# Kernel optimization log

Measured on AMD Instinct MI355X. Metric: run time of the kernel, lower is better.

Reference implementation:

```python
import jax, jax.numpy as jnp
import numpy as np

N_NODES = 100000
N_EDGES = 3200000
IN_DIM = 512
OUT_DIM = 3


def _sage_conv(x, src, dst, ll_w, ll_b, lr_w):
    # PyG SAGEConv (mean aggr): out = lin_l(mean_{j in N(i)} x_j) + lin_r(x_i)
    n = x.shape[0]
    msgs = x[src]                                            # [E, d_in]
    agg = jax.ops.segment_sum(msgs, dst, num_segments=n)      # [N, d_in]
    cnt = jax.ops.segment_sum(jnp.ones((src.shape[0],), x.dtype), dst, num_segments=n)
    mean = agg / jnp.maximum(cnt, 1.0)[:, None]
    return mean @ ll_w + ll_b + x @ lr_w


def setup_inputs() -> dict:
    key = jax.random.key(0)
    ks = jax.random.split(key, 16)
    d = {}
    d["x"] = jax.random.normal(ks[0], (N_NODES, IN_DIM), dtype=jnp.float32)
    d["edge_index"] = jax.random.randint(ks[1], (2, N_EDGES), 0, N_NODES, dtype=jnp.int64)
    s = lambda fan_in: 1.0 / np.sqrt(fan_in)
    d["fc1_w"] = jax.random.uniform(ks[2], (IN_DIM, 16), jnp.float32, -s(IN_DIM), s(IN_DIM))
    d["fc1_b"] = jax.random.uniform(ks[3], (16,), jnp.float32, -s(IN_DIM), s(IN_DIM))
    d["conv1_ll_w"] = jax.random.uniform(ks[4], (16, 32), jnp.float32, -s(16), s(16))
    d["conv1_ll_b"] = jnp.zeros((32,), jnp.float32)
    d["conv1_lr_w"] = jax.random.uniform(ks[5], (16, 32), jnp.float32, -s(16), s(16))
    d["conv2_ll_w"] = jax.random.uniform(ks[6], (32, 16), jnp.float32, -s(32), s(32))
    d["conv2_ll_b"] = jnp.zeros((16,), jnp.float32)
    d["conv2_lr_w"] = jax.random.uniform(ks[7], (32, 16), jnp.float32, -s(32), s(32))
    d["fc2_w"] = jax.random.uniform(ks[8], (16, OUT_DIM), jnp.float32, -s(16), s(16))
    d["fc2_b"] = jax.random.uniform(ks[9], (OUT_DIM,), jnp.float32, -s(16), s(16))
    return d


def reference(x, edge_index, fc1_w, fc1_b, conv1_ll_w, conv1_ll_b, conv1_lr_w,
              conv2_ll_w, conv2_ll_b, conv2_lr_w, fc2_w, fc2_b):
    src, dst = edge_index[0], edge_index[1]
    h = jax.nn.relu(x @ fc1_w + fc1_b)                              # [N, 16]
    h = jax.nn.relu(_sage_conv(h, src, dst, conv1_ll_w, conv1_ll_b, conv1_lr_w))  # [N, 32]
    h = jax.nn.relu(_sage_conv(h, src, dst, conv2_ll_w, conv2_ll_b, conv2_lr_w))  # [N, 16]
    h = h @ fc2_w + fc2_b                                           # [N, 3]
    gsi = jax.nn.sigmoid(h[:, 1])
    mxi = jax.nn.sigmoid(h[:, 2])
    fsi = jax.nn.relu(h[:, 0]) + gsi
    return jnp.stack([fsi, gsi, mxi], axis=1)
```

## Files before the change

### kernel.cpp

```cpp
#include <hip/hip_runtime.h>
#include <math.h>

#define N_NODES 100000
#define N_EDGES 3200000
#define BSHIFT 8
#define NPB 256
#define BMASK (NPB - 1)
#define NB 391
#define CAP 10240
#define STG_BLOCKS 512
#define FC1_BLOCKS 2048
#define NTILES 6250

typedef __attribute__((ext_vector_type(8))) short short8v;
typedef __attribute__((ext_vector_type(4))) float f32x4;
typedef __attribute__((address_space(3))) unsigned lds_u32;
typedef const __attribute__((address_space(1))) unsigned glb_u32;

__device__ inline unsigned cvt_pk_bf16(float a, float b) {
  unsigned r;
  asm("v_cvt_pk_bf16_f32 %0, %1, %2" : "=v"(r) : "v"(a), "v"(b));
  return r;
}
__device__ inline unsigned short f32_to_bf16(float f) {
  union { float f; unsigned u; } v; v.f = f;
  unsigned r = v.u + 0x7fff + ((v.u >> 16) & 1);
  return (unsigned short)(r >> 16);
}
__device__ inline float bf16_to_f32(unsigned short h) {
  union { unsigned u; float f; } v; v.u = ((unsigned)h) << 16;
  return v.f;
}

__global__ __launch_bounds__(256) void fc1_stage_kernel(
    const float* __restrict__ x, const float* __restrict__ w,
    const float* __restrict__ b, unsigned short* __restrict__ h1,
    const int* __restrict__ src, const int* __restrict__ dst,
    int* __restrict__ gcur, int* __restrict__ staged) {
  __shared__ __align__(16) char smem[53248];

  if (blockIdx.x >= STG_BLOCKS) {
    float* tile = (float*)smem;
    short8v (*wlds)[64] = (short8v(*)[64])(smem + 32768);
    f32x4* pbuf = (f32x4*)(smem + 49152);
    const int tid = threadIdx.x;
    const int lane = tid & 63;
    const int wib = tid >> 6;
    const int o = lane & 15;
    const int kb = lane >> 4;

    for (int i = tid; i < 2048; i += 256)
      ((float4*)tile)[i] = ((const float4*)w)[i];
    __syncthreads();
    for (int idx = tid; idx < 4096; idx += 256) {
      const int s = idx >> 8, ln = (idx >> 2) & 63, j = idx & 3;
      const int lkb = ln >> 4, lo = ln & 15;
      const int k = s * 32 + lkb * 8 + 2 * j;
      ((unsigned*)&wlds[s][ln])[j] =
          cvt_pk_bf16(tile[k * 16 + lo], tile[(k + 1) * 16 + lo]);
    }
    __syncthreads();

    const float bias = b[o];
    const int fcb = blockIdx.x - STG_BLOCKS;

    for (int tileid = fcb; tileid < NTILES; tileid += FC1_BLOCKS) {
      const float* xbase = x + (size_t)tileid * 8192;
#pragma unroll
      for (int i = 0; i < 8; ++i) {
        const int c = wib * 8 + i;
        const int r = c >> 1;
        const int off = (c & 1) * 1024 + lane * 16;
        const int goff = off ^ ((r & 7) << 5);
        __builtin_amdgcn_global_load_lds(
            (glb_u32*)(xbase + r * 512 + (goff >> 2)),
            (lds_u32*)((char*)tile + (size_t)c * 1024 + lane * 16) - lane * 4,
            16, 0, 0);
      }
      __syncthreads();

      f32x4 c4 = {0.f, 0.f, 0.f, 0.f};
#pragma unroll
      for (int ss = 0; ss < 4; ++ss) {
        const int s = wib * 4 + ss;
        const int cb = (s * 128 + kb * 32) ^ ((o & 7) << 5);
        const char* p = (const char*)tile + o * 2048 + cb;
        const float4 a0 = *(const float4*)p;
        const float4 a1 = *(const float4*)(p + 16);
        union { unsigned u[4]; short8v v; } fa;
        fa.u[0] = cvt_pk_bf16(a0.x, a0.y);
        fa.u[1] = cvt_pk_bf16(a0.z, a0.w);
        fa.u[2] = cvt_pk_bf16(a1.x, a1.y);
        fa.u[3] = cvt_pk_bf16(a1.z, a1.w);
        c4 = __builtin_amdgcn_mfma_f32_16x16x32_bf16(fa.v, wlds[s][lane], c4,
                                                     0, 0, 0);
      }
      pbuf[wib * 64 + lane] = c4;
      __syncthreads();
      if (wib == 0) {
        const f32x4 p0 = pbuf[lane];
        const f32x4 p1 = pbuf[64 + lane];
        const f32x4 p2 = pbuf[128 + lane];
        const f32x4 p3 = pbuf[192 + lane];
        const int rbase = tileid * 16 + (lane >> 4) * 4;
#pragma unroll
        for (int j = 0; j < 4; ++j) {
          const float vj = (p0[j] + p1[j]) + (p2[j] + p3[j]);
          h1[(size_t)(rbase + j) * 16 + o] =
              f32_to_bf16(fmaxf(vj + bias, 0.f));
        }
      }
      __syncthreads();
    }
  } else {
    int* hist = (int*)smem;
    int* base = (int*)(smem + 2048);
    const int tid = threadIdx.x;
    for (int i = tid; i < NB; i += 256) hist[i] = 0;
    __syncthreads();

    const int sb = blockIdx.x;
    const int per = (N_EDGES + STG_BLOCKS - 1) / STG_BLOCKS;
    const int e0 = sb * per;
    const int e1 = min(e0 + per, N_EDGES);

    for (int e = e0 + tid; e < e1; e += 256) {
      atomicAdd(&hist[dst[e] >> BSHIFT], 1);
    }
    __syncthreads();
    for (int bkt = tid; bkt < NB; bkt += 256) {
      int h = hist[bkt];
      base[bkt] = (h > 0) ? atomicAdd(&gcur[bkt], h) : 0;
      hist[bkt] = 0;
    }
    __syncthreads();
    for (int e = e0 + tid; e < e1; e += 256) {
      int d = dst[e];
      int s = src[e];
      int bkt = d >> BSHIFT;
      int pos = base[bkt] + atomicAdd(&hist[bkt], 1);
      if (pos < CAP) staged[bkt * CAP + pos] = (s << 8) | (d & BMASK);
    }
  }
}

__global__ __launch_bounds__(256) void finalize_kernel(
    int* __restrict__ staged, const int* __restrict__ gcur,
    int* __restrict__ offs, int* __restrict__ cnt) {
  __shared__ int ed[CAP];
  __shared__ int lcnt[NPB];
  __shared__ int lofs[NPB];
  __shared__ int sc[256];
  const int bkt = blockIdx.x, tid = threadIdx.x;
  const int nE = min(gcur[bkt], CAP);
  const int base = bkt * CAP;
  for (int e = tid; e < nE; e += 256) ed[e] = staged[base + e];
  lcnt[tid] = 0;
  __syncthreads();
  for (int e = tid; e < nE; e += 256) atomicAdd(&lcnt[ed[e] & BMASK], 1);
  __syncthreads();
  const int v = lcnt[tid];
  sc[tid] = v;
  __syncthreads();
  for (int d = 1; d < 256; d <<= 1) {
    int add = (tid >= d) ? sc[tid - d] : 0;
    __syncthreads();
    sc[tid] += add;
    __syncthreads();
  }
  const int excl = sc[tid] - v;
  lofs[tid] = excl;
  const int g = bkt * NPB + tid;
  if (g < N_NODES) {
    offs[g] = base + excl;
    cnt[g] = v;
  }
  lcnt[tid] = 0;
  __syncthreads();
  for (int e = tid; e < nE; e += 256) {
    int u = ed[e];
    int dl = u & BMASK;
    int pos = lofs[dl] + atomicAdd(&lcnt[dl], 1);
    staged[base + pos] = u >> 8;
  }
}

__global__ __launch_bounds__(256) void conv1_kernel(
    const unsigned short* __restrict__ h1, const int* __restrict__ csr,
    const int* __restrict__ offs, const int* __restrict__ cnt,
    const float* __restrict__ llw, const float* __restrict__ llb,
    const float* __restrict__ lrw, const float* __restrict__ c2llw,
    float* __restrict__ h2, unsigned short* __restrict__ t2) {
  __shared__ float wl[512], wr[512], w2c[512];
  __shared__ float bb[32];
  for (int idx = threadIdx.x; idx < 512; idx += 256) {
    const int k = idx >> 5, jj = idx & 31;
    const int sj = 4 * ((jj >> 2) ^ (k >> 2)) + (jj & 3);
    wl[k * 32 + sj] = llw[idx];
    wr[k * 32 + sj] = lrw[idx];
    w2c[idx] = c2llw[idx];
  }
  if (threadIdx.x < 32) bb[threadIdx.x] = llb[threadIdx.x];
  __syncthreads();

  const int tid = blockIdx.x * 256 + threadIdx.x;
  const int i = tid >> 3;
  if (i >= N_NODES) return;
  const int t8 = threadIdx.x & 7;
  const int gg = t8 >> 2;
  const int t = t8 & 3;
  const int start = offs[i], deg = cnt[i];

  float4 acc = make_float4(0.f, 0.f, 0.f, 0.f);
  int e = gg;
  for (; e + 6 < deg; e += 8) {
    const int s0 = csr[start + e];
    const int s1 = csr[start + e + 2];
    const int s2 = csr[start + e + 4];
    const int s3 = csr[start + e + 6];
    ushort4 a0 = *(const ushort4*)(h1 + (size_t)s0 * 16 + t * 4);
    ushort4 a1 = *(const ushort4*)(h1 + (size_t)s1 * 16 + t * 4);
    ushort4 a2 = *(const ushort4*)(h1 + (size_t)s2 * 16 + t * 4);
    ushort4 a3 = *(const ushort4*)(h1 + (size_t)s3 * 16 + t * 4);
    acc.x += (bf16_to_f32(a0.x) + bf16_to_f32(a1.x)) +
             (bf16_to_f32(a2.x) + bf16_to_f32(a3.x));
    acc.y += (bf16_to_f32(a0.y) + bf16_to_f32(a1.y)) +
             (bf16_to_f32(a2.y) + bf16_to_f32(a3.y));
    acc.z += (bf16_to_f32(a0.z) + bf16_to_f32(a1.z)) +
             (bf16_to_f32(a2.z) + bf16_to_f32(a3.z));
    acc.w += (bf16_to_f32(a0.w) + bf16_to_f32(a1.w)) +
             (bf16_to_f32(a2.w) + bf16_to_f32(a3.w));
  }
  for (; e < deg; e += 2) {
    const int s = csr[start + e];
    ushort4 a = *(const ushort4*)(h1 + (size_t)s * 16 + t * 4);
    acc.x += bf16_to_f32(a.x); acc.y += bf16_to_f32(a.y);
    acc.z += bf16_to_f32(a.z); acc.w += bf16_to_f32(a.w);
  }
  acc.x += __shfl_xor(acc.x, 4, 64);
  acc.y += __shfl_xor(acc.y, 4, 64);
  acc.z += __shfl_xor(acc.z, 4, 64);
  acc.w += __shfl_xor(acc.w, 4, 64);

  const float inv = 1.f / (float)(deg > 0 ? deg : 1);
  const ushort4 selfu = *(const ushort4*)(h1 + (size_t)i * 16 + t * 4);
  const float mk[4] = {acc.x * inv, acc.y * inv, acc.z * inv, acc.w * inv};
  const float sk[4] = {bf16_to_f32(selfu.x), bf16_to_f32(selfu.y),
                       bf16_to_f32(selfu.z), bf16_to_f32(selfu.w)};

  float4 p[8];
#pragma unroll
  for (int q = 0; q < 8; ++q) p[q] = make_float4(0.f, 0.f, 0.f, 0.f);
#pragma unroll
  for (int j = 0; j < 4; ++j) {
    const int k = 4 * t + j;
#pragma unroll
    for (int q = 0; q < 8; ++q) {
      const int qs = 4 * (q ^ t);
      float4 w4l = *(const float4*)&wl[k * 32 + qs];
      float4 w4r = *(const float4*)&wr[k * 32 + qs];
      p[q].x += mk[j] * w4l.x + sk[j] * w4r.x;
      p[q].y += mk[j] * w4l.y + sk[j] * w4r.y;
      p[q].z += mk[j] * w4l.z + sk[j] * w4r.z;
      p[q].w += mk[j] * w4l.w + sk[j] * w4r.w;
    }
  }
#pragma unroll
  for (int mask = 1; mask <= 2; mask <<= 1) {
#pragma unroll
    for (int q = 0; q < 8; ++q) {
      p[q].x += __shfl_xor(p[q].x, mask, 64);
      p[q].y += __shfl_xor(p[q].y, mask, 64);
      p[q].z += __shfl_xor(p[q].z, mask, 64);
      p[q].w += __shfl_xor(p[q].w, mask, 64);
    }
  }
  float o[32];
#pragma unroll
  for (int q = 0; q < 8; ++q) {
    o[4 * q + 0] = fmaxf(p[q].x + bb[4 * q + 0], 0.f);
    o[4 * q + 1] = fmaxf(p[q].y + bb[4 * q + 1], 0.f);
    o[4 * q + 2] = fmaxf(p[q].z + bb[4 * q + 2], 0.f);
    o[4 * q + 3] = fmaxf(p[q].w + bb[4 * q + 3], 0.f);
  }
  *(float4*)(h2 + (size_t)i * 32 + 4 * t8) =
      make_float4(o[4 * t8], o[4 * t8 + 1], o[4 * t8 + 2], o[4 * t8 + 3]);
  float t0 = 0.f, t1 = 0.f;
#pragma unroll
  for (int k = 0; k < 32; ++k) {
    const float ok = o[k];
    t0 += ok * w2c[k * 16 + 2 * t8];
    t1 += ok * w2c[k * 16 + 2 * t8 + 1];
  }
  *(unsigned*)(t2 + (size_t)i * 16 + 2 * t8) = cvt_pk_bf16(t0, t1);
}

__global__ __launch_bounds__(256) void conv2_kernel(
    const unsigned short* __restrict__ t2, const float* __restrict__ h2,
    const int* __restrict__ csr, const int* __restrict__ offs,
    const int* __restrict__ cnt, const float* __restrict__ llb,
    const float* __restrict__ lrw, const float* __restrict__ fc2w,
    const float* __restrict__ fc2b, float* __restrict__ out) {
  __shared__ float wr[512];
  __shared__ float bb[16];
  __shared__ float w2[48];
  __shared__ float b2[3];
  for (int idx = threadIdx.x; idx < 512; idx += 256) {
    const int k = idx >> 4, jj = idx & 15;
    const int sj = 4 * ((jj >> 2) ^ ((k >> 2) & 3)) + (jj & 3);
    wr[k * 16 + sj] = lrw[idx];
  }
  if (threadIdx.x < 16) bb[threadIdx.x] = llb[threadIdx.x];
  else if (threadIdx.x >= 64 && threadIdx.x < 112) w2[threadIdx.x - 64] = fc2w[threadIdx.x - 64];
  else if (threadIdx.x >= 128 && threadIdx.x < 131) b2[threadIdx.x - 128] = fc2b[threadIdx.x - 128];
  __syncthreads();

  const int tid = blockIdx.x * 256 + threadIdx.x;
  const int i = tid >> 3;
  if (i >= N_NODES) return;
  const int t8 = threadIdx.x & 7;
  const int gg = t8 >> 2;
  const int t = t8 & 3;
  const int start = offs[i], deg = cnt[i];

  float4 acc = make_float4(0.f, 0.f, 0.f, 0.f);
  int e = gg;
  for (; e + 6 < deg; e += 8) {
    const int s0 = csr[start + e];
    const int s1 = csr[start + e + 2];
    const int s2 = csr[start + e + 4];
    const int s3 = csr[start + e + 6];
    ushort4 a0 = *(const ushort4*)(t2 + (size_t)s0 * 16 + t * 4);
    ushort4 a1 = *(const ushort4*)(t2 + (size_t)s1 * 16 + t * 4);
    ushort4 a2 = *(const ushort4*)(t2 + (size_t)s2 * 16 + t * 4);
    ushort4 a3 = *(const ushort4*)(t2 + (size_t)s3 * 16 + t * 4);
    acc.x += (bf16_to_f32(a0.x) + bf16_to_f32(a1.x)) +
             (bf16_to_f32(a2.x) + bf16_to_f32(a3.x));
    acc.y += (bf16_to_f32(a0.y) + bf16_to_f32(a1.y)) +
             (bf16_to_f32(a2.y) + bf16_to_f32(a3.y));
    acc.z += (bf16_to_f32(a0.z) + bf16_to_f32(a1.z)) +
             (bf16_to_f32(a2.z) + bf16_to_f32(a3.z));
    acc.w += (bf16_to_f32(a0.w) + bf16_to_f32(a1.w)) +
             (bf16_to_f32(a2.w) + bf16_to_f32(a3.w));
  }
  for (; e < deg; e += 2) {
    const int s = csr[start + e];
    ushort4 a = *(const ushort4*)(t2 + (size_t)s * 16 + t * 4);
    acc.x += bf16_to_f32(a.x); acc.y += bf16_to_f32(a.y);
    acc.z += bf16_to_f32(a.z); acc.w += bf16_to_f32(a.w);
  }
  acc.x += __shfl_xor(acc.x, 4, 64);
  acc.y += __shfl_xor(acc.y, 4, 64);
  acc.z += __shfl_xor(acc.z, 4, 64);
  acc.w += __shfl_xor(acc.w, 4, 64);

  const float inv = 1.f / (float)(deg > 0 ? deg : 1);
  const float4 s0v = *(const float4*)(h2 + (size_t)i * 32 + 4 * t8);
  const float sk[4] = {s0v.x, s0v.y, s0v.z, s0v.w};
  float4 p[4];
#pragma unroll
  for (int q = 0; q < 4; ++q) p[q] = make_float4(0.f, 0.f, 0.f, 0.f);
#pragma unroll
  for (int kk = 0; kk < 4; ++kk) {
    const int k = 4 * t8 + kk;
    const float s = sk[kk];
#pragma unroll
    for (int q = 0; q < 4; ++q) {
      const int qs = 4 * (q ^ (t8 & 3));
      const float4 wv = *(const float4*)&wr[k * 16 + qs];
      p[q].x += s * wv.x; p[q].y += s * wv.y;
      p[q].z += s * wv.z; p[q].w += s * wv.w;
    }
  }
  if (gg == 0) {
    p[t].x += acc.x * inv; p[t].y += acc.y * inv;
    p[t].z += acc.z * inv; p[t].w += acc.w * inv;
  }
#pragma unroll
  for (int mask = 1; mask <= 4; mask <<= 1) {
#pragma unroll
    for (int q = 0; q < 4; ++q) {
      p[q].x += __shfl_xor(p[q].x, mask, 64);
      p[q].y += __shfl_xor(p[q].y, mask, 64);
      p[q].z += __shfl_xor(p[q].z, mask, 64);
      p[q].w += __shfl_xor(p[q].w, mask, 64);
    }
  }
  if (t8 < 3) {
    float f[16];
#pragma unroll
    for (int q = 0; q < 4; ++q) {
      f[4 * q + 0] = fmaxf(p[q].x + bb[4 * q + 0], 0.f);
      f[4 * q + 1] = fmaxf(p[q].y + bb[4 * q + 1], 0.f);
      f[4 * q + 2] = fmaxf(p[q].z + bb[4 * q + 2], 0.f);
      f[4 * q + 3] = fmaxf(p[q].w + bb[4 * q + 3], 0.f);
    }
    float v0 = b2[0], v1 = b2[1], v2 = b2[2];
#pragma unroll
    for (int k = 0; k < 16; ++k) {
      v0 += f[k] * w2[k * 3 + 0];
      v1 += f[k] * w2[k * 3 + 1];
      v2 += f[k] * w2[k * 3 + 2];
    }
    float gsi = 1.f / (1.f + expf(-v1));
    float mxi = 1.f / (1.f + expf(-v2));
    float fsi = fmaxf(v0, 0.f) + gsi;
    float rv = (t8 == 0) ? fsi : ((t8 == 1) ? gsi : mxi);
    out[(size_t)i * 3 + t8] = rv;
  }
}

extern "C" void kernel_launch(void* const* d_in, const int* in_sizes, int n_in,
                              void* d_out, int out_size, void* d_ws, size_t ws_size,
                              hipStream_t stream) {
  const float* x = (const float*)d_in[0];
  const int* ei = (const int*)d_in[1];
  const float* fc1w = (const float*)d_in[2];
  const float* fc1b = (const float*)d_in[3];
  const float* c1llw = (const float*)d_in[4];
  const float* c1llb = (const float*)d_in[5];
  const float* c1lrw = (const float*)d_in[6];
  const float* c2llw = (const float*)d_in[7];
  const float* c2llb = (const float*)d_in[8];
  const float* c2lrw = (const float*)d_in[9];
  const float* fc2w = (const float*)d_in[10];
  const float* fc2b = (const float*)d_in[11];
  float* outp = (float*)d_out;
  const int* src = ei;
  const int* dst = ei + N_EDGES;

  char* ws = (char*)d_ws;
  unsigned short* h1 = (unsigned short*)ws;  ws += (size_t)N_NODES * 16 * 2;
  float* h2 = (float*)ws;                    ws += (size_t)N_NODES * 32 * 4;
  unsigned short* t2 = (unsigned short*)ws;  ws += (size_t)N_NODES * 16 * 2;
  int* staged = (int*)ws;                    ws += (size_t)NB * CAP * 4;
  int* gcur = (int*)ws;                      ws += (size_t)NB * 4;
  int* offs = (int*)ws;                      ws += (size_t)N_NODES * 4;
  int* cnt = (int*)ws;                       ws += (size_t)N_NODES * 4;
  (void)ws_size; (void)n_in; (void)in_sizes; (void)out_size;

  hipMemsetAsync(gcur, 0, (size_t)NB * 4, stream);
  fc1_stage_kernel<<<STG_BLOCKS + FC1_BLOCKS, 256, 0, stream>>>(
      x, fc1w, fc1b, h1, src, dst, gcur, staged);
  finalize_kernel<<<NB, 256, 0, stream>>>(staged, gcur, offs, cnt);
  conv1_kernel<<<(N_NODES * 8 + 255) / 256, 256, 0, stream>>>(
      h1, staged, offs, cnt, c1llw, c1llb, c1lrw, c2llw, h2, t2);
  conv2_kernel<<<(N_NODES * 8 + 255) / 256, 256, 0, stream>>>(
      t2, h2, staged, offs, cnt, c2llb, c2lrw, fc2w, fc2b, outp);
}
```

Baseline: 215.4 us.

## Give each wave its own fc1 tile to remove block barriers and partial reductions

The fc1 path now has two waves per block, each owning a private 32KB LDS tile and processing an entire 16-row tile with all 16 K-steps, instead of four waves splitting K and reducing partials through LDS. This removes the per-tile __syncthreads and the partial-sum buffer, and uses per-wave vmcnt waits instead. In exchange the block shares 80KB of LDS, which may reduce occupancy, and half the waves in fc1 blocks sit idle. The staging blocks also get the larger shared allocation, which may hurt their occupancy.

```diff
diff --git a/kernel.cpp b/kernel.cpp
--- a/kernel.cpp
+++ b/kernel.cpp
@@ -37,80 +37,76 @@
     const float* __restrict__ b, unsigned short* __restrict__ h1,
     const int* __restrict__ src, const int* __restrict__ dst,
     int* __restrict__ gcur, int* __restrict__ staged) {
-  __shared__ __align__(16) char smem[53248];
+  __shared__ __align__(16) char smem[81920];
 
   if (blockIdx.x >= STG_BLOCKS) {
-    float* tile = (float*)smem;
-    short8v (*wlds)[64] = (short8v(*)[64])(smem + 32768);
-    f32x4* pbuf = (f32x4*)(smem + 49152);
+    short8v (*wlds)[64] = (short8v(*)[64])smem;
+    char* tiles = smem + 16384;
     const int tid = threadIdx.x;
     const int lane = tid & 63;
     const int wib = tid >> 6;
     const int o = lane & 15;
     const int kb = lane >> 4;
 
+    float* scratch = (float*)tiles;
     for (int i = tid; i < 2048; i += 256)
-      ((float4*)tile)[i] = ((const float4*)w)[i];
-    __syncthreads();
-    for (int idx = tid; idx < 4096; idx += 256) {
+      ((float4*)scratch)[i] = ((const float4*)w)[i];
+    __syncthreads();
+    unsigned wpk[16];
+    for (int idx = tid, n = 0; idx < 4096; idx += 256, ++n) {
       const int s = idx >> 8, ln = (idx >> 2) & 63, j = idx & 3;
       const int lkb = ln >> 4, lo = ln & 15;
       const int k = s * 32 + lkb * 8 + 2 * j;
-      ((unsigned*)&wlds[s][ln])[j] =
-          cvt_pk_bf16(tile[k * 16 + lo], tile[(k + 1) * 16 + lo]);
-    }
-    __syncthreads();
-
-    const float bias = b[o];
-    const int fcb = blockIdx.x - STG_BLOCKS;
-
-    for (int tileid = fcb; tileid < NTILES; tileid += FC1_BLOCKS) {
-      const float* xbase = x + (size_t)tileid * 8192;
-#pragma unroll
-      for (int i = 0; i < 8; ++i) {
-        const int c = wib * 8 + i;
-        const int r = c >> 1;
-        const int off = (c & 1) * 1024 + lane * 16;
-        const int goff = off ^ ((r & 7) << 5);
-        __builtin_amdgcn_global_load_lds(
-            (glb_u32*)(xbase + r * 512 + (goff >> 2)),
-            (lds_u32*)((char*)tile + (size_t)c * 1024 + lane * 16) - lane * 4,
-            16, 0, 0);
-      }
-      __syncthreads();
-
-      f32x4 c4 = {0.f, 0.f, 0.f, 0.f};
-#pragma unroll
-      for (int ss = 0; ss < 4; ++ss) {
-        const int s = wib * 4 + ss;
-        const int cb = (s * 128 + kb * 32) ^ ((o & 7) << 5);
-        const char* p = (const char*)tile + o * 2048 + cb;
-        const float4 a0 = *(const float4*)p;
-        const float4 a1 = *(const float4*)(p + 16);
-        union { unsigned u[4]; short8v v; } fa;
-        fa.u[0] = cvt_pk_bf16(a0.x, a0.y);
-        fa.u[1] = cvt_pk_bf16(a0.z, a0.w);
-        fa.u[2] = cvt_pk_bf16(a1.x, a1.y);
-        fa.u[3] = cvt_pk_bf16(a1.z, a1.w);
-        c4 = __builtin_amdgcn_mfma_f32_16x16x32_bf16(fa.v, wlds[s][lane], c4,
-                                                     0, 0, 0);
-      }
-      pbuf[wib * 64 + lane] = c4;
-      __syncthreads();
-      if (wib == 0) {
-        const f32x4 p0 = pbuf[lane];
-        const f32x4 p1 = pbuf[64 + lane];
-        const f32x4 p2 = pbuf[128 + lane];
-        const f32x4 p3 = pbuf[192 + lane];
-        const int rbase = tileid * 16 + (lane >> 4) * 4;
+      wpk[n] = cvt_pk_bf16(scratch[k * 16 + lo], scratch[(k + 1) * 16 + lo]);
+    }
+    __syncthreads();
+    for (int idx = tid, n = 0; idx < 4096; idx += 256, ++n) {
+      ((unsigned*)wlds)[((idx >> 2) << 2) + (idx & 3)] = wpk[n];
+    }
+    __syncthreads();
+
+    if (wib < 2) {
+      char* mybuf = tiles + (size_t)wib * 32768;
+      const float bias = b[o];
+      const int wid = (blockIdx.x - STG_BLOCKS) * 2 + wib;
+
+      for (int tl = wid; tl < NTILES; tl += FC1_BLOCKS * 2) {
+        const float* xbase = x + (size_t)tl * 8192;
+#pragma unroll
+        for (int i = 0; i < 32; ++i) {
+          const int r = i >> 1;
+          const int off = (i & 1) * 1024 + lane * 16;
+          const int goff = off ^ ((r & 7) << 5);
+          __builtin_amdgcn_global_load_lds(
+              (glb_u32*)(xbase + r * 512 + (goff >> 2)),
+              (lds_u32*)(mybuf + (size_t)i * 1024 + lane * 16) - lane * 4,
+              16, 0, 0);
+        }
+        asm volatile("s_waitcnt vmcnt(0)" ::: "memory");
+        __builtin_amdgcn_sched_barrier(0);
+
+        f32x4 c4 = {0.f, 0.f, 0.f, 0.f};
+#pragma unroll
+        for (int s = 0; s < 16; ++s) {
+          const int cb = (s * 128 + kb * 32) ^ ((o & 7) << 5);
+          const char* p = mybuf + o * 2048 + cb;
+          const float4 a0 = *(const float4*)p;
+          const float4 a1 = *(const float4*)(p + 16);
+          union { unsigned u[4]; short8v v; } fa;
+          fa.u[0] = cvt_pk_bf16(a0.x, a0.y);
+          fa.u[1] = cvt_pk_bf16(a0.z, a0.w);
+          fa.u[2] = cvt_pk_bf16(a1.x, a1.y);
+          fa.u[3] = cvt_pk_bf16(a1.z, a1.w);
+          c4 = __builtin_amdgcn_mfma_f32_16x16x32_bf16(fa.v, wlds[s][lane],
+                                                       c4, 0, 0, 0);
+        }
+        const int rbase = tl * 16 + (lane >> 4) * 4;
 #pragma unroll
         for (int j = 0; j < 4; ++j) {
-          const float vj = (p0[j] + p1[j]) + (p2[j] + p3[j]);
           h1[(size_t)(rbase + j) * 16 + o] =
-              f32_to_bf16(fmaxf(vj + bias, 0.f));
+              f32_to_bf16(fmaxf(c4[j] + bias, 0.f));
         }
       }
-      __syncthreads();
     }
   } else {
     int* hist = (int*)smem;
```

Result: slower. 220.3 us (+2.3%).
